# Optimization experiments

Measured on AMD Instinct MI355X. Metric: run time of the kernel, lower is better.

## Reference

```python
import jax, jax.numpy as jnp
import numpy as np

EPS = 1e-8

def l2norm(x, axis=-1, eps=EPS):
    n = jnp.sqrt(jnp.sum(x * x, axis=axis, keepdims=True)) + eps
    return x / n

def setup_inputs() -> dict:
    key = jax.random.key(0)
    k1, k2, k3, k4 = jax.random.split(key, 4)
    B, Q, S, D, SIM = 512, 64, 36, 1024, 256
    query = jax.random.normal(k1, (B, Q, D), dtype=jnp.float32)
    context = jax.random.normal(k2, (B, S, D), dtype=jnp.float32)
    matrix = jax.random.uniform(k3, (B, Q, D), dtype=jnp.float32)
    W = jax.random.normal(k4, (SIM, D), dtype=jnp.float32) * 0.02
    b = jnp.zeros((SIM,), dtype=jnp.float32)
    return {"query": query, "context": context, "matrix": matrix,
            "W": W, "b": b, "smooth": 9}

def reference(query, context, matrix, W, b, smooth):
    # cross_attention
    q = query * matrix                                  # (B,Q,D)
    attn = jnp.einsum('bsd,bqd->bsq', context, q)       # (B,S,Q)
    attn = jnp.where(attn > 0, attn, 0.1 * attn)        # LeakyReLU(0.1)
    attn = l2norm(attn, axis=-1)                        # l2norm over Q
    attn = jnp.swapaxes(attn, 1, 2)                     # (B,Q,S)
    attn = jax.nn.softmax(attn * smooth, axis=2)        # temperature softmax over S
    wcontext = jnp.einsum('bqs,bsd->bqd', attn, context)
    wcontext = l2norm(wcontext, axis=-1)
    # Alignment_vector: squared diff -> linear -> l2norm
    sim_rep = (query - wcontext) ** 2                   # (B,Q,D)
    sim_rep = jnp.einsum('bqd,kd->bqk', sim_rep, W) + b # (B,Q,SIM)
    return l2norm(sim_rep, axis=-1)
```

## Files before the change

### kernel.cpp

```cpp
#include <hip/hip_runtime.h>
#include <hip/hip_bf16.h>

#define BB 512
#define QQ 64
#define SS 36
#define DD 1024
#define SIM 256

typedef unsigned short u16x8 __attribute__((ext_vector_type(8)));
typedef unsigned short u16x4 __attribute__((ext_vector_type(4)));
typedef __bf16 bf16x8 __attribute__((ext_vector_type(8)));
typedef float f32x4 __attribute__((ext_vector_type(4)));
typedef unsigned short us;

__device__ __forceinline__ us f2bf(float f) {
  unsigned u = __float_as_uint(f);
  u += 0x7FFFu + ((u >> 16) & 1u);
  return (us)(u >> 16);
}
__device__ __forceinline__ float bf2f(us h) {
  return __uint_as_float(((unsigned)h) << 16);
}

__global__ __launch_bounds__(256) void k0_w16(const float* __restrict__ W,
                                              us* __restrict__ W16) {
  int i = blockIdx.x * 256 + threadIdx.x;
  float4 v = ((const float4*)W)[i];
  ushort4 p;
  p.x = f2bf(v.x); p.y = f2bf(v.y); p.z = f2bf(v.z); p.w = f2bf(v.w);
  ((ushort4*)W16)[i] = p;
}

__global__ __launch_bounds__(256) void k1_attn(
    const float* __restrict__ query, const float* __restrict__ context,
    const float* __restrict__ matrix, const int* __restrict__ smoothp,
    us* __restrict__ attnBF, us* __restrict__ Gws) {
  __shared__ __align__(16) char smem1[30464];
  us* qmL = (us*)smem1;
  us* ctxL = (us*)(smem1 + 17408);
  float* sc = (float*)smem1;

  const int t = threadIdx.x;
  const int bb = blockIdx.x;
  const int lane = t & 63, w = t >> 6;
  const int ml = lane & 15, kg = lane >> 4;
  const float smf = (float)smoothp[0];

  f32x4 acc[3];
#pragma unroll
  for (int mt = 0; mt < 3; ++mt) acc[mt] = (f32x4){0.f, 0.f, 0.f, 0.f};
  f32x4 accg[3];
#pragma unroll
  for (int j = 0; j < 3; ++j) accg[j] = (f32x4){0.f, 0.f, 0.f, 0.f};

  for (int ch = 0; ch < 8; ++ch) {
    const int d0 = ch * 128;
#pragma unroll
    for (int i = 0; i < 4; ++i) {
      int idx = t + 256 * i;
      int row = idx >> 4, c8 = idx & 15;
      const float4* gq = (const float4*)&query[((size_t)bb * QQ + row) * DD + d0 + c8 * 8];
      const float4* gm = (const float4*)&matrix[((size_t)bb * QQ + row) * DD + d0 + c8 * 8];
      float4 a0 = gq[0], a1 = gq[1], m0 = gm[0], m1 = gm[1];
      u16x8 pk;
      pk[0] = f2bf(a0.x * m0.x); pk[1] = f2bf(a0.y * m0.y);
      pk[2] = f2bf(a0.z * m0.z); pk[3] = f2bf(a0.w * m0.w);
      pk[4] = f2bf(a1.x * m1.x); pk[5] = f2bf(a1.y * m1.y);
      pk[6] = f2bf(a1.z * m1.z); pk[7] = f2bf(a1.w * m1.w);
      *(u16x8*)&qmL[row * 136 + c8 * 8] = pk;
    }
#pragma unroll
    for (int i = 0; i < 3; ++i) {
      int idx = t + 256 * i;
      int row = idx >> 4, c8 = idx & 15;
      u16x8 pk = (u16x8){0, 0, 0, 0, 0, 0, 0, 0};
      if (row < 36) {
        const float4* gc = (const float4*)&context[((size_t)bb * SS + row) * DD + d0 + c8 * 8];
        float4 a0 = gc[0], a1 = gc[1];
        pk[0] = f2bf(a0.x); pk[1] = f2bf(a0.y); pk[2] = f2bf(a0.z); pk[3] = f2bf(a0.w);
        pk[4] = f2bf(a1.x); pk[5] = f2bf(a1.y); pk[6] = f2bf(a1.z); pk[7] = f2bf(a1.w);
      }
      *(u16x8*)&ctxL[row * 136 + c8 * 8] = pk;
    }
    __syncthreads();
#pragma unroll
    for (int ks = 0; ks < 4; ++ks) {
      const int ko = ks * 32 + kg * 8;
      bf16x8 bfrag = __builtin_bit_cast(bf16x8, *(const u16x8*)&qmL[(w * 16 + ml) * 136 + ko]);
      bf16x8 af0 = __builtin_bit_cast(bf16x8, *(const u16x8*)&ctxL[(0 + ml) * 136 + ko]);
      bf16x8 af1 = __builtin_bit_cast(bf16x8, *(const u16x8*)&ctxL[(16 + ml) * 136 + ko]);
      bf16x8 af2 = __builtin_bit_cast(bf16x8, *(const u16x8*)&ctxL[(32 + ml) * 136 + ko]);
      acc[0] = __builtin_amdgcn_mfma_f32_16x16x32_bf16(af0, bfrag, acc[0], 0, 0, 0);
      acc[1] = __builtin_amdgcn_mfma_f32_16x16x32_bf16(af1, bfrag, acc[1], 0, 0, 0);
      acc[2] = __builtin_amdgcn_mfma_f32_16x16x32_bf16(af2, bfrag, acc[2], 0, 0, 0);
      if (w < 3) {
        bf16x8 ai = __builtin_bit_cast(bf16x8, *(const u16x8*)&ctxL[(w * 16 + ml) * 136 + ko]);
        accg[0] = __builtin_amdgcn_mfma_f32_16x16x32_bf16(ai, af0, accg[0], 0, 0, 0);
        accg[1] = __builtin_amdgcn_mfma_f32_16x16x32_bf16(ai, af1, accg[1], 0, 0, 0);
        accg[2] = __builtin_amdgcn_mfma_f32_16x16x32_bf16(ai, af2, accg[2], 0, 0, 0);
      }
    }
    __syncthreads();
  }

  if (w < 3) {
#pragma unroll
    for (int j = 0; j < 3; ++j)
#pragma unroll
      for (int ii = 0; ii < 4; ++ii)
        Gws[(size_t)bb * 2304 + (w * 16 + kg * 4 + ii) * 48 + j * 16 + ml] = f2bf(accg[j][ii]);
  }
#pragma unroll
  for (int mt = 0; mt < 3; ++mt)
#pragma unroll
    for (int ii = 0; ii < 4; ++ii) {
      float v = acc[mt][ii];
      v = v > 0.f ? v : 0.1f * v;
      sc[(mt * 16 + kg * 4 + ii) * 68 + w * 16 + ml] = v;
    }
  __syncthreads();

  if (t < 36) {
    float ssum = 0.f;
    for (int qi = 0; qi < 64; ++qi) { float v = sc[t * 68 + qi]; ssum = fmaf(v, v, ssum); }
    float rn = 1.f / (sqrtf(ssum) + 1e-8f);
    for (int qi = 0; qi < 64; ++qi) sc[t * 68 + qi] *= rn;
  }
  __syncthreads();

  if (t < 64) {
    float mx = -1e30f;
    for (int s2 = 0; s2 < 36; ++s2) mx = fmaxf(mx, sc[s2 * 68 + t]);
    float sum = 0.f;
    float ev[36];
    for (int s2 = 0; s2 < 36; ++s2) {
      float e = __expf((sc[s2 * 68 + t] - mx) * smf);
      ev[s2] = e;
      sum += e;
    }
    float rs = 1.f / sum;
    size_t base = (size_t)bb * (QQ * SS) + t * SS;
#pragma unroll
    for (int s2 = 0; s2 < 36; ++s2) attnBF[base + s2] = f2bf(ev[s2] * rs);
  }
}

template <bool USE_W16>
__global__ __launch_bounds__(512, 4) void k2_fused(
    const float* __restrict__ query, const float* __restrict__ context,
    const float* __restrict__ Wm, const float* __restrict__ bvec,
    const us* __restrict__ attnBF, const us* __restrict__ Gws,
    const us* __restrict__ W16, float* __restrict__ out) {
  __shared__ __align__(16) char smem[49664];
  us* P16s = (us*)smem;
  us* ctxTs = (us*)(smem + 9216);
  us* A16s = (us*)(smem + 28672);
  us* Gf16L = (us*)(smem + 28672);
  float* biasL = (float*)(smem + 46080);
  float* rnL = (float*)(smem + 47104);
  float* rsum = (float*)(smem + 47360);

  const int t = threadIdx.x, bb = blockIdx.x;
  const int lane = t & 63, w = t >> 6;
  const int ml = lane & 15, kg = lane >> 4;

  for (int idx = t; idx < 2304; idx += 512) ((unsigned*)P16s)[idx] = 0;
  for (int idx = t; idx < 1728; idx += 512) ((unsigned*)Gf16L)[idx] = 0;
  for (int idx = t; idx < 1792; idx += 512) {
    int r = idx / 14, c = idx - r * 14;
    *(unsigned*)&ctxTs[r * 76 + 36 + c * 2] = 0;
  }
  if (t < 256) biasL[t] = bvec[t];
  __syncthreads();
  for (int idx = t; idx < 1152; idx += 512) {
    int q = idx / 18, c2 = idx - q * 18;
    *(unsigned*)&P16s[q * 72 + c2 * 2] = ((const unsigned*)attnBF)[(size_t)bb * 1152 + idx];
  }
  for (int idx = t; idx < 1152; idx += 512) {
    int r = idx / 24, c2 = idx - r * 24;
    *(unsigned*)&Gf16L[r * 72 + c2 * 2] = ((const unsigned*)Gws)[(size_t)bb * 1152 + idx];
  }
  __syncthreads();

  if (w < 3) {
    f32x4 accv[4];
#pragma unroll
    for (int mt = 0; mt < 4; ++mt) accv[mt] = (f32x4){0.f, 0.f, 0.f, 0.f};
#pragma unroll
    for (int ks = 0; ks < 2; ++ks) {
      const int ko = ks * 32 + kg * 8;
      bf16x8 gfr = __builtin_bit_cast(bf16x8, *(const u16x8*)&Gf16L[(w * 16 + ml) * 72 + ko]);
#pragma unroll
      for (int mt = 0; mt < 4; ++mt) {
        bf16x8 pf = __builtin_bit_cast(bf16x8, *(const u16x8*)&P16s[(mt * 16 + ml) * 72 + ko]);
        accv[mt] = __builtin_amdgcn_mfma_f32_16x16x32_bf16(pf, gfr, accv[mt], 0, 0, 0);
      }
    }
#pragma unroll
    for (int mt = 0; mt < 4; ++mt)
#pragma unroll
      for (int ii = 0; ii < 4; ++ii) {
        int q = mt * 16 + kg * 4 + ii;
        float vv = accv[mt][ii] * bf2f(P16s[q * 72 + w * 16 + ml]);
        vv += __shfl_xor(vv, 1);
        vv += __shfl_xor(vv, 2);
        vv += __shfl_xor(vv, 4);
        vv += __shfl_xor(vv, 8);
        if (ml == 0) rsum[q * 4 + w] = vv;
      }
  }
  __syncthreads();
  if (t < 64) {
    float s2 = rsum[t * 4] + rsum[t * 4 + 1] + rsum[t * 4 + 2];
    rnL[t] = 1.f / (sqrtf(s2) + 1e-8f);
  }

  f32x4 accs[4][2];
#pragma unroll
  for (int mt = 0; mt < 4; ++mt)
#pragma unroll
    for (int ntl = 0; ntl < 2; ++ntl) accs[mt][ntl] = (f32x4){0.f, 0.f, 0.f, 0.f};

  for (int ch = 0; ch < 8; ++ch) {
    const int d0 = ch * 128;
    for (int idx = t; idx < 1152; idx += 512) {
      int d = idx & 127, s0 = (idx >> 7) * 4;
      const float* cp = &context[((size_t)bb * SS + s0) * DD + d0 + d];
      u16x4 pk;
      pk[0] = f2bf(cp[0]);
      pk[1] = f2bf(cp[DD]);
      pk[2] = f2bf(cp[2 * DD]);
      pk[3] = f2bf(cp[3 * DD]);
      *(u16x4*)&ctxTs[d * 76 + s0] = pk;
    }
    __syncthreads();
    f32x4 aw[4];
#pragma unroll
    for (int mt = 0; mt < 4; ++mt) aw[mt] = (f32x4){0.f, 0.f, 0.f, 0.f};
#pragma unroll
    for (int ks = 0; ks < 2; ++ks) {
      const int ko = ks * 32 + kg * 8;
      u16x4 blo = *(const u16x4*)&ctxTs[(w * 16 + ml) * 76 + ko];
      u16x4 bhi = *(const u16x4*)&ctxTs[(w * 16 + ml) * 76 + ko + 4];
      bf16x8 bfr = __builtin_bit_cast(bf16x8, __builtin_shufflevector(blo, bhi, 0, 1, 2, 3, 4, 5, 6, 7));
#pragma unroll
      for (int mt = 0; mt < 4; ++mt) {
        bf16x8 af = __builtin_bit_cast(bf16x8, *(const u16x8*)&P16s[(mt * 16 + ml) * 72 + ko]);
        aw[mt] = __builtin_amdgcn_mfma_f32_16x16x32_bf16(af, bfr, aw[mt], 0, 0, 0);
      }
    }
#pragma unroll
    for (int mt = 0; mt < 4; ++mt)
#pragma unroll
      for (int ii = 0; ii < 4; ++ii) {
        int q = mt * 16 + kg * 4 + ii;
        float qv = query[((size_t)bb * QQ + q) * DD + d0 + w * 16 + ml];
        float av = qv - aw[mt][ii] * rnL[q];
        A16s[q * 136 + w * 16 + ml] = f2bf(av * av);
      }
    __syncthreads();
#pragma unroll
    for (int ks = 0; ks < 4; ++ks) {
      const int ko = ks * 32 + kg * 8;
      bf16x8 bfr[2];
#pragma unroll
      for (int ntl = 0; ntl < 2; ++ntl) {
        const size_t wrow = (size_t)(w * 32 + ntl * 16 + ml);
        if constexpr (USE_W16) {
          bfr[ntl] = __builtin_bit_cast(bf16x8, *(const u16x8*)&W16[wrow * DD + d0 + ko]);
        } else {
          const float4* wp = (const float4*)&Wm[wrow * DD + d0 + ko];
          float4 x = wp[0], y = wp[1];
          u16x8 pk;
          pk[0] = f2bf(x.x); pk[1] = f2bf(x.y); pk[2] = f2bf(x.z); pk[3] = f2bf(x.w);
          pk[4] = f2bf(y.x); pk[5] = f2bf(y.y); pk[6] = f2bf(y.z); pk[7] = f2bf(y.w);
          bfr[ntl] = __builtin_bit_cast(bf16x8, pk);
        }
      }
#pragma unroll
      for (int mt = 0; mt < 4; ++mt) {
        bf16x8 af = __builtin_bit_cast(bf16x8, *(const u16x8*)&A16s[(mt * 16 + ml) * 136 + ko]);
#pragma unroll
        for (int ntl = 0; ntl < 2; ++ntl)
          accs[mt][ntl] = __builtin_amdgcn_mfma_f32_16x16x32_bf16(af, bfr[ntl], accs[mt][ntl], 0, 0, 0);
      }
    }
    __syncthreads();
  }

#pragma unroll
  for (int mt = 0; mt < 4; ++mt)
#pragma unroll
    for (int ii = 0; ii < 4; ++ii) {
      int q = mt * 16 + kg * 4 + ii;
      float partial = 0.f;
#pragma unroll
      for (int ntl = 0; ntl < 2; ++ntl) {
        int col = w * 32 + ntl * 16 + ml;
        float v = accs[mt][ntl][ii] + biasL[col];
        partial = fmaf(v, v, partial);
      }
      partial += __shfl_xor(partial, 1);
      partial += __shfl_xor(partial, 2);
      partial += __shfl_xor(partial, 4);
      partial += __shfl_xor(partial, 8);
      if (ml == 0) rsum[q * 9 + w] = partial;
    }
  __syncthreads();
  if (t < 64) {
    float ssum = 0.f;
#pragma unroll
    for (int w2 = 0; w2 < 8; ++w2) ssum += rsum[t * 9 + w2];
    rnL[t] = 1.f / (sqrtf(ssum) + 1e-8f);
  }
  __syncthreads();
#pragma unroll
  for (int mt = 0; mt < 4; ++mt)
#pragma unroll
    for (int ntl = 0; ntl < 2; ++ntl)
#pragma unroll
      for (int ii = 0; ii < 4; ++ii) {
        int q = mt * 16 + kg * 4 + ii;
        int col = w * 32 + ntl * 16 + ml;
        float v = accs[mt][ntl][ii] + biasL[col];
        out[((size_t)bb * QQ + q) * SIM + col] = v * rnL[q];
      }
}

extern "C" void kernel_launch(void* const* d_in, const int* in_sizes, int n_in,
                              void* d_out, int out_size, void* d_ws, size_t ws_size,
                              hipStream_t stream) {
  const float* query = (const float*)d_in[0];
  const float* context = (const float*)d_in[1];
  const float* matrix = (const float*)d_in[2];
  const float* Wm = (const float*)d_in[3];
  const float* bvec = (const float*)d_in[4];
  const int* smoothp = (const int*)d_in[5];
  float* out = (float*)d_out;

  const size_t attnB = (size_t)BB * QQ * SS * 2;
  us* attnBF = (us*)d_ws;
  us* Gws = (us*)((char*)d_ws + attnB);
  us* W16 = (us*)((char*)d_ws + 2 * attnB);
  const bool useW16 = ws_size >= 2 * attnB + (size_t)SIM * DD * 2;

  k1_attn<<<dim3(BB), dim3(256), 0, stream>>>(query, context, matrix, smoothp, attnBF, Gws);
  if (useW16) {
    k0_w16<<<dim3(SIM * DD / 1024), dim3(256), 0, stream>>>(Wm, W16);
    k2_fused<true><<<dim3(BB), dim3(512), 0, stream>>>(query, context, Wm, bvec, attnBF, Gws, W16, out);
  } else {
    k2_fused<false><<<dim3(BB), dim3(512), 0, stream>>>(query, context, Wm, bvec, attnBF, Gws, W16, out);
  }
}
```

Measured before the change: 169.1 us.

## Fuse attention and projection kernels into one 512-thread kernel per batch

Merges the attention-score kernel into the fused projection kernel, so the softmax weights and the context Gram matrix stay in shared memory and no longer make a round trip through a global workspace. Inside the first phase the score MFMAs and the Gram MFMAs now run on separate wavefronts (waves 0-3 and 4-6) instead of being done together by four waves. This removes one launch and the global traffic for the intermediates. In exchange, shared memory grows to about 62KB per block, which may lower occupancy relative to the launch bound of 4 blocks.

```diff
diff --git a/kernel.cpp b/kernel.cpp
--- a/kernel.cpp
+++ b/kernel.cpp
@@ -31,33 +31,45 @@
   ((ushort4*)W16)[i] = p;
 }
 
-__global__ __launch_bounds__(256) void k1_attn(
+template <bool USE_W16>
+__global__ __launch_bounds__(512, 4) void k_fused(
     const float* __restrict__ query, const float* __restrict__ context,
-    const float* __restrict__ matrix, const int* __restrict__ smoothp,
-    us* __restrict__ attnBF, us* __restrict__ Gws) {
-  __shared__ __align__(16) char smem1[30464];
-  us* qmL = (us*)smem1;
-  us* ctxL = (us*)(smem1 + 17408);
-  float* sc = (float*)smem1;
-
-  const int t = threadIdx.x;
-  const int bb = blockIdx.x;
+    const float* __restrict__ matrix, const float* __restrict__ Wm,
+    const float* __restrict__ bvec, const int* __restrict__ smoothp,
+    const us* __restrict__ W16, float* __restrict__ out) {
+  __shared__ __align__(16) char smem[63232];
+  us* qmL = (us*)smem;
+  us* ctxL = (us*)(smem + 17408);
+  float* sc = (float*)(smem + 30464);
+  us* ctxTs = (us*)smem;
+  us* A16s = (us*)(smem + 19456);
+  us* P16s = (us*)(smem + 43520);
+  us* Gf16L = (us*)(smem + 52736);
+  float* biasL = (float*)(smem + 59648);
+  float* rnL = (float*)(smem + 60672);
+  float* rsum = (float*)(smem + 60928);
+
+  const int t = threadIdx.x, bb = blockIdx.x;
   const int lane = t & 63, w = t >> 6;
   const int ml = lane & 15, kg = lane >> 4;
   const float smf = (float)smoothp[0];
 
-  f32x4 acc[3];
-#pragma unroll
-  for (int mt = 0; mt < 3; ++mt) acc[mt] = (f32x4){0.f, 0.f, 0.f, 0.f};
-  f32x4 accg[3];
-#pragma unroll
-  for (int j = 0; j < 3; ++j) accg[j] = (f32x4){0.f, 0.f, 0.f, 0.f};
+  for (int idx = t; idx < 2304; idx += 512) ((unsigned*)P16s)[idx] = 0;
+  for (int idx = t; idx < 1728; idx += 512) ((unsigned*)Gf16L)[idx] = 0;
+  if (t < 256) biasL[t] = bvec[t];
+
+  f32x4 acc[3], gacc[3];
+#pragma unroll
+  for (int j = 0; j < 3; ++j) {
+    acc[j] = (f32x4){0.f, 0.f, 0.f, 0.f};
+    gacc[j] = (f32x4){0.f, 0.f, 0.f, 0.f};
+  }
 
   for (int ch = 0; ch < 8; ++ch) {
     const int d0 = ch * 128;
 #pragma unroll
-    for (int i = 0; i < 4; ++i) {
-      int idx = t + 256 * i;
+    for (int i = 0; i < 2; ++i) {
+      int idx = t + 512 * i;
       int row = idx >> 4, c8 = idx & 15;
       const float4* gq = (const float4*)&query[((size_t)bb * QQ + row) * DD + d0 + c8 * 8];
       const float4* gm = (const float4*)&matrix[((size_t)bb * QQ + row) * DD + d0 + c8 * 8];
@@ -69,10 +81,17 @@
       pk[6] = f2bf(a1.z * m1.z); pk[7] = f2bf(a1.w * m1.w);
       *(u16x8*)&qmL[row * 136 + c8 * 8] = pk;
     }
-#pragma unroll
-    for (int i = 0; i < 3; ++i) {
-      int idx = t + 256 * i;
-      int row = idx >> 4, c8 = idx & 15;
+    {
+      int row = t >> 4, c8 = t & 15;
+      const float4* gc = (const float4*)&context[((size_t)bb * SS + row) * DD + d0 + c8 * 8];
+      float4 a0 = gc[0], a1 = gc[1];
+      u16x8 pk;
+      pk[0] = f2bf(a0.x); pk[1] = f2bf(a0.y); pk[2] = f2bf(a0.z); pk[3] = f2bf(a0.w);
+      pk[4] = f2bf(a1.x); pk[5] = f2bf(a1.y); pk[6] = f2bf(a1.z); pk[7] = f2bf(a1.w);
+      *(u16x8*)&ctxL[row * 136 + c8 * 8] = pk;
+    }
+    if (t < 256) {
+      int row = 32 + (t >> 4), c8 = t & 15;
       u16x8 pk = (u16x8){0, 0, 0, 0, 0, 0, 0, 0};
       if (row < 36) {
         const float4* gc = (const float4*)&context[((size_t)bb * SS + row) * DD + d0 + c8 * 8];
@@ -86,38 +105,41 @@
 #pragma unroll
     for (int ks = 0; ks < 4; ++ks) {
       const int ko = ks * 32 + kg * 8;
-      bf16x8 bfrag = __builtin_bit_cast(bf16x8, *(const u16x8*)&qmL[(w * 16 + ml) * 136 + ko]);
-      bf16x8 af0 = __builtin_bit_cast(bf16x8, *(const u16x8*)&ctxL[(0 + ml) * 136 + ko]);
-      bf16x8 af1 = __builtin_bit_cast(bf16x8, *(const u16x8*)&ctxL[(16 + ml) * 136 + ko]);
-      bf16x8 af2 = __builtin_bit_cast(bf16x8, *(const u16x8*)&ctxL[(32 + ml) * 136 + ko]);
-      acc[0] = __builtin_amdgcn_mfma_f32_16x16x32_bf16(af0, bfrag, acc[0], 0, 0, 0);
-      acc[1] = __builtin_amdgcn_mfma_f32_16x16x32_bf16(af1, bfrag, acc[1], 0, 0, 0);
-      acc[2] = __builtin_amdgcn_mfma_f32_16x16x32_bf16(af2, bfrag, acc[2], 0, 0, 0);
-      if (w < 3) {
-        bf16x8 ai = __builtin_bit_cast(bf16x8, *(const u16x8*)&ctxL[(w * 16 + ml) * 136 + ko]);
-        accg[0] = __builtin_amdgcn_mfma_f32_16x16x32_bf16(ai, af0, accg[0], 0, 0, 0);
-        accg[1] = __builtin_amdgcn_mfma_f32_16x16x32_bf16(ai, af1, accg[1], 0, 0, 0);
-        accg[2] = __builtin_amdgcn_mfma_f32_16x16x32_bf16(ai, af2, accg[2], 0, 0, 0);
-      }
-    }
-    __syncthreads();
-  }
-
-  if (w < 3) {
+      if (w < 4) {
+        bf16x8 bq = __builtin_bit_cast(bf16x8, *(const u16x8*)&qmL[(w * 16 + ml) * 136 + ko]);
+#pragma unroll
+        for (int mt = 0; mt < 3; ++mt) {
+          bf16x8 af = __builtin_bit_cast(bf16x8, *(const u16x8*)&ctxL[(mt * 16 + ml) * 136 + ko]);
+          acc[mt] = __builtin_amdgcn_mfma_f32_16x16x32_bf16(af, bq, acc[mt], 0, 0, 0);
+        }
+      } else if (w < 7) {
+        bf16x8 ai = __builtin_bit_cast(bf16x8, *(const u16x8*)&ctxL[((w - 4) * 16 + ml) * 136 + ko]);
+#pragma unroll
+        for (int j = 0; j < 3; ++j) {
+          bf16x8 aj = __builtin_bit_cast(bf16x8, *(const u16x8*)&ctxL[(j * 16 + ml) * 136 + ko]);
+          gacc[j] = __builtin_amdgcn_mfma_f32_16x16x32_bf16(ai, aj, gacc[j], 0, 0, 0);
+        }
+      }
+    }
+    __syncthreads();
+  }
+
+  if (w < 4) {
+#pragma unroll
+    for (int mt = 0; mt < 3; ++mt)
+#pragma unroll
+      for (int ii = 0; ii < 4; ++ii) {
+        float v = acc[mt][ii];
+        v = v > 0.f ? v : 0.1f * v;
+        sc[(mt * 16 + kg * 4 + ii) * 68 + w * 16 + ml] = v;
+      }
+  } else if (w < 7) {
 #pragma unroll
     for (int j = 0; j < 3; ++j)
 #pragma unroll
       for (int ii = 0; ii < 4; ++ii)
-        Gws[(size_t)bb * 2304 + (w * 16 + kg * 4 + ii) * 48 + j * 16 + ml] = f2bf(accg[j][ii]);
-  }
-#pragma unroll
-  for (int mt = 0; mt < 3; ++mt)
-#pragma unroll
-    for (int ii = 0; ii < 4; ++ii) {
-      float v = acc[mt][ii];
-      v = v > 0.f ? v : 0.1f * v;
-      sc[(mt * 16 + kg * 4 + ii) * 68 + w * 16 + ml] = v;
-    }
+        Gf16L[((w - 4) * 16 + kg * 4 + ii) * 72 + j * 16 + ml] = f2bf(gacc[j][ii]);
+  }
   __syncthreads();
 
   if (t < 36) {
@@ -139,46 +161,8 @@
       sum += e;
     }
     float rs = 1.f / sum;
-    size_t base = (size_t)bb * (QQ * SS) + t * SS;
-#pragma unroll
-    for (int s2 = 0; s2 < 36; ++s2) attnBF[base + s2] = f2bf(ev[s2] * rs);
-  }
-}
-
-template <bool USE_W16>
-__global__ __launch_bounds__(512, 4) void k2_fused(
-    const float* __restrict__ query, const float* __restrict__ context,
-    const float* __restrict__ Wm, const float* __restrict__ bvec,
-    const us* __restrict__ attnBF, const us* __restrict__ Gws,
-    const us* __restrict__ W16, float* __restrict__ out) {
-  __shared__ __align__(16) char smem[49664];
-  us* P16s = (us*)smem;
-  us* ctxTs = (us*)(smem + 9216);
-  us* A16s = (us*)(smem + 28672);
-  us* Gf16L = (us*)(smem + 28672);
-  float* biasL = (float*)(smem + 46080);
-  float* rnL = (float*)(smem + 47104);
-  float* rsum = (float*)(smem + 47360);
-
-  const int t = threadIdx.x, bb = blockIdx.x;
-  const int lane = t & 63, w = t >> 6;
-  const int ml = lane & 15, kg = lane >> 4;
-
-  for (int idx = t; idx < 2304; idx += 512) ((unsigned*)P16s)[idx] = 0;
-  for (int idx = t; idx < 1728; idx += 512) ((unsigned*)Gf16L)[idx] = 0;
-  for (int idx = t; idx < 1792; idx += 512) {
-    int r = idx / 14, c = idx - r * 14;
-    *(unsigned*)&ctxTs[r * 76 + 36 + c * 2] = 0;
-  }
-  if (t < 256) biasL[t] = bvec[t];
-  __syncthreads();
-  for (int idx = t; idx < 1152; idx += 512) {
-    int q = idx / 18, c2 = idx - q * 18;
-    *(unsigned*)&P16s[q * 72 + c2 * 2] = ((const unsigned*)attnBF)[(size_t)bb * 1152 + idx];
-  }
-  for (int idx = t; idx < 1152; idx += 512) {
-    int r = idx / 24, c2 = idx - r * 24;
-    *(unsigned*)&Gf16L[r * 72 + c2 * 2] = ((const unsigned*)Gws)[(size_t)bb * 1152 + idx];
+#pragma unroll
+    for (int s2 = 0; s2 < 36; ++s2) P16s[t * 72 + s2] = f2bf(ev[s2] * rs);
   }
   __syncthreads();
 
@@ -214,6 +198,11 @@
     float s2 = rsum[t * 4] + rsum[t * 4 + 1] + rsum[t * 4 + 2];
     rnL[t] = 1.f / (sqrtf(s2) + 1e-8f);
   }
+  for (int idx = t; idx < 1792; idx += 512) {
+    int r = idx / 14, c = idx - r * 14;
+    *(unsigned*)&ctxTs[r * 76 + 36 + c * 2] = 0;
+  }
+  __syncthreads();
 
   f32x4 accs[4][2];
 #pragma unroll
@@ -338,17 +327,15 @@
   const int* smoothp = (const int*)d_in[5];
   float* out = (float*)d_out;
 
-  const size_t attnB = (size_t)BB * QQ * SS * 2;
-  us* attnBF = (us*)d_ws;
-  us* Gws = (us*)((char*)d_ws + attnB);
-  us* W16 = (us*)((char*)d_ws + 2 * attnB);
-  const bool useW16 = ws_size >= 2 * attnB + (size_t)SIM * DD * 2;
-
-  k1_attn<<<dim3(BB), dim3(256), 0, stream>>>(query, context, matrix, smoothp, attnBF, Gws);
+  us* W16 = (us*)d_ws;
+  const bool useW16 = ws_size >= (size_t)SIM * DD * 2;
+
   if (useW16) {
     k0_w16<<<dim3(SIM * DD / 1024), dim3(256), 0, stream>>>(Wm, W16);
-    k2_fused<true><<<dim3(BB), dim3(512), 0, stream>>>(query, context, Wm, bvec, attnBF, Gws, W16, out);
+    k_fused<true><<<dim3(BB), dim3(512), 0, stream>>>(query, context, matrix, Wm,
+                                                      bvec, smoothp, W16, out);
   } else {
-    k2_fused<false><<<dim3(BB), dim3(512), 0, stream>>>(query, context, Wm, bvec, attnBF, Gws, W16, out);
-  }
-}
+    k_fused<false><<<dim3(BB), dim3(512), 0, stream>>>(query, context, matrix, Wm,
+                                                       bvec, smoothp, W16, out);
+  }
+}
```

After: 160.6 us. 1.05x faster.
